# Kernel optimization log

Measured on AMD Instinct MI355X. Metric: run time of the kernel, lower is better.

The kernel has to match this reference:

```python
import jax, jax.numpy as jnp
import numpy as np

OLD = (32, 32)   # fine grid coord_dims
NEW = (16, 16)   # coarse grid (dims // 2)
N_ORDERS = 6     # multi-indices of total order <= 2 in 2 coords


def lin_resize(x, new_size, axis):
    # 1D linear interpolation along `axis`, align_corners=True (matches F.interpolate)
    old = x.shape[axis]
    pos = jnp.arange(new_size, dtype=x.dtype) * ((old - 1) / (new_size - 1))
    lo = jnp.clip(jnp.floor(pos).astype(jnp.int32), 0, old - 2)
    w = pos - lo.astype(x.dtype)
    xl = jnp.take(x, lo, axis=axis)
    xh = jnp.take(x, lo + 1, axis=axis)
    shp = [1] * x.ndim
    shp[axis] = new_size
    w = w.reshape(shp)
    return xl * (1.0 - w) + xh * w


def bilinear_resize(x, new_hw):
    # separable bilinear, align_corners=True; x is [..., H, W]
    x = lin_resize(x, new_hw[0], x.ndim - 2)
    return lin_resize(x, new_hw[1], x.ndim - 1)


def setup_inputs():
    key = jax.random.key(0)
    ks = jax.random.split(key, 6)
    B = 32                      # bs * n_ind_dim = 8 * 4
    G = OLD[0] * OLD[1]         # fine grid size = 1024
    m, n = 2048, 1536           # coarse constraints x coarse vars (16*16*6)
    return {
        "coeffs": jax.random.normal(ks[0], (B, G, N_ORDERS), jnp.float32),
        "rhs": jax.random.normal(ks[1], (B, G), jnp.float32),
        "steps_x": jax.random.uniform(ks[2], (B, OLD[0] - 1), jnp.float32),
        "steps_y": jax.random.uniform(ks[3], (B, OLD[1] - 1), jnp.float32),
        "A": jax.random.normal(ks[4], (B, m, n), jnp.float32) * 0.05,
        "A_rhs": jax.random.normal(ks[5], (B, m), jnp.float32),
    }


def reference(coeffs, rhs, steps_x, steps_y, A, A_rhs):
    B = coeffs.shape[0]
    new_G = NEW[0] * NEW[1]

    # --- downsample_coeffs: [B,G,O] -> [B,O,H,W] -> bilinear -> [B,newG,O]
    c = coeffs.transpose(0, 2, 1).reshape(B, N_ORDERS, OLD[0], OLD[1])
    c = bilinear_resize(c, NEW)
    new_coeffs = c.reshape(B, N_ORDERS, new_G).transpose(0, 2, 1)

    # --- downsample_rhs: [B,G] -> [B,1,H,W] -> bilinear -> [B,newG]
    r = bilinear_resize(rhs.reshape(B, 1, OLD[0], OLD[1]), NEW)
    new_rhs = r.reshape(B, new_G)

    # --- downsample_steps: drop last, pairwise sum
    nsx = steps_x[:, :-1].reshape(B, OLD[0] // 2 - 1, 2).sum(axis=-1)
    nsy = steps_y[:, :-1].reshape(B, OLD[1] // 2 - 1, 2).sum(axis=-1)

    # --- make_AtA (coarsest path: dense bmm) ---
    AtA = jnp.einsum('bmn,bmk->bnk', A, A)           # At @ A, [B,n,n]
    AtPrhs = jnp.einsum('bmn,bm->bn', A, A_rhs)      # At @ rhs
    D = jnp.sum(A * A, axis=1)                       # diag(AtA) = column sums of squares

    # --- L/U split (get_tril): L = cols <= rows, U = cols > rows ---
    n = AtA.shape[-1]
    ridx = jnp.arange(n)
    lmask = ridx[:, None] >= ridx[None, :]
    L = jnp.where(lmask, AtA, jnp.zeros((), AtA.dtype))
    U = jnp.where(lmask, jnp.zeros((), AtA.dtype), AtA)

    return (new_coeffs, new_rhs, nsx, nsy, AtA, AtPrhs, D, L, U)
```

## Files before the change

kernel.cpp:

```cpp
#include <hip/hip_runtime.h>
#include <math.h>

#define NB 32
#define M 2048
#define N 1536
#define NORD 6

#define OFF_COEFFS 0
#define OFF_RHS    49152
#define OFF_NSX    57344
#define OFF_NSY    57824
#define OFF_ATA    58304
#define OFF_ATPRHS 75555776
#define OFF_D      75604928
#define OFF_L      75654080
#define OFF_U      151151552
#define SMALL_TOTAL 58304

typedef short short8v __attribute__((ext_vector_type(8)));
typedef float f32x4 __attribute__((ext_vector_type(4)));

__device__ __forceinline__ void gload16(const void* g, void* l) {
    __builtin_amdgcn_global_load_lds(
        (const __attribute__((address_space(1))) void*)g,
        (__attribute__((address_space(3))) void*)l, 16, 0, 0);
}

__device__ __forceinline__ uint rtn_bf16(float x) {
    uint u = __float_as_uint(x);
    return (u + 0x7fffu + ((u >> 16) & 1u)) >> 16;
}

__device__ __forceinline__ void nts(float v, float* p) {
    __builtin_nontemporal_store(v, p);
}
__device__ __forceinline__ void nts4(f32x4 v, float* p) {
    __builtin_nontemporal_store(v, (f32x4*)p);
}

__global__ void small_kernel(const float* __restrict__ coeffs,
                             const float* __restrict__ rhs,
                             const float* __restrict__ sx,
                             const float* __restrict__ sy,
                             float* __restrict__ out) {
    int idx = blockIdx.x * blockDim.x + threadIdx.x;
    if (idx >= SMALL_TOTAL) return;
    const float scale = 31.0f / 15.0f;
    if (idx < 49152) {
        int b = idx / 1536;
        int rem = idx % 1536;
        int gp = rem / 6;
        int o  = rem % 6;
        int yy = gp / 16, xx = gp % 16;
        float py = (float)yy * scale;
        int ly = (int)floorf(py); if (ly > 30) ly = 30;
        float wy = py - (float)ly;
        float px = (float)xx * scale;
        int lx = (int)floorf(px); if (lx > 30) lx = 30;
        float wx = px - (float)lx;
        const float* base = coeffs + (size_t)b * 1024 * NORD;
        float v00 = base[(ly * 32 + lx) * NORD + o];
        float v01 = base[(ly * 32 + lx + 1) * NORD + o];
        float v10 = base[((ly + 1) * 32 + lx) * NORD + o];
        float v11 = base[((ly + 1) * 32 + lx + 1) * NORD + o];
        float a  = v00 * (1.0f - wy) + v10 * wy;
        float bb = v01 * (1.0f - wy) + v11 * wy;
        out[OFF_COEFFS + idx] = a * (1.0f - wx) + bb * wx;
    } else if (idx < 57344) {
        int j = idx - 49152;
        int b = j / 256;
        int gp = j % 256;
        int yy = gp / 16, xx = gp % 16;
        float py = (float)yy * scale;
        int ly = (int)floorf(py); if (ly > 30) ly = 30;
        float wy = py - (float)ly;
        float px = (float)xx * scale;
        int lx = (int)floorf(px); if (lx > 30) lx = 30;
        float wx = px - (float)lx;
        const float* base = rhs + (size_t)b * 1024;
        float v00 = base[ly * 32 + lx];
        float v01 = base[ly * 32 + lx + 1];
        float v10 = base[(ly + 1) * 32 + lx];
        float v11 = base[(ly + 1) * 32 + lx + 1];
        float a  = v00 * (1.0f - wy) + v10 * wy;
        float bb = v01 * (1.0f - wy) + v11 * wy;
        out[OFF_RHS + j] = a * (1.0f - wx) + bb * wx;
    } else if (idx < 57824) {
        int j = idx - 57344;
        int b = j / 15, k = j % 15;
        out[OFF_NSX + j] = sx[b * 31 + 2 * k] + sx[b * 31 + 2 * k + 1];
    } else {
        int j = idx - 57824;
        int b = j / 15, k = j % 15;
        out[OFF_NSY + j] = sy[b * 31 + 2 * k] + sy[b * 31 + 2 * k + 1];
    }
}

__global__ __launch_bounds__(256) void split_kernel(const float* __restrict__ A,
                                                    const float* __restrict__ Arhs,
                                                    ushort* __restrict__ Ahi,
                                                    float2* __restrict__ part) {
    int bid = blockIdx.x;
    int q  = bid & 3;
    int cb = (bid >> 2) % 6;
    int b  = bid / 24;
    int t  = threadIdx.x;
    int col = cb * 256 + t;
    const float* Ab = A + (size_t)b * M * N;
    const float* rb = Arhs + (size_t)b * M;
    uint4* Hp = (uint4*)Ahi;
    float s1 = 0.0f, s2 = 0.0f;
    for (int oct = q * 64; oct < q * 64 + 64; ++oct) {
        uint hw[4];
#pragma unroll
        for (int j = 0; j < 4; ++j) {
            float a0 = Ab[(size_t)(oct * 8 + 2 * j) * N + col];
            float a1 = Ab[(size_t)(oct * 8 + 2 * j + 1) * N + col];
            float r0 = rb[oct * 8 + 2 * j];
            float r1 = rb[oct * 8 + 2 * j + 1];
            s1 = fmaf(a0, r0, s1); s1 = fmaf(a1, r1, s1);
            s2 = fmaf(a0, a0, s2); s2 = fmaf(a1, a1, s2);
            hw[j] = rtn_bf16(a0) | (rtn_bf16(a1) << 16);
        }
        Hp[(size_t)(b * 256 + oct) * N + col] = make_uint4(hw[0], hw[1], hw[2], hw[3]);
    }
    part[(size_t)q * (NB * 6 * 256) + (size_t)(b * 6 + cb) * 256 + t] = make_float2(s1, s2);
}

__global__ __launch_bounds__(256) void reduce_kernel(const float2* __restrict__ part,
                                                     float* __restrict__ out) {
    int idx = blockIdx.x * 256 + threadIdx.x;
    float s1 = 0.0f, s2 = 0.0f;
#pragma unroll
    for (int q = 0; q < 4; ++q) {
        float2 p = part[(size_t)q * (NB * 6 * 256) + idx];
        s1 += p.x; s2 += p.y;
    }
    out[OFF_ATPRHS + idx] = s1;
    out[OFF_D + idx] = s2;
}

#define SYRK_BLOCKS (NB * 78)

__global__ __launch_bounds__(256, 4) void syrk3_kernel(const ushort* __restrict__ Ahi,
                                                       float* __restrict__ out) {
    __shared__ ushort lds[2][1024 * 8];

    int bid = blockIdx.x;
    int swz = (bid % 8) * (SYRK_BLOCKS / 8) + bid / 8;
    int b = swz / 78;
    int p = swz % 78;
    int ti = 0;
    while ((ti + 1) * (ti + 2) / 2 <= p) ++ti;
    int tj = p - ti * (ti + 1) / 2;
    bool diag = (ti == tj);
    int i0 = ti * 128, j0 = tj * 128;

    int t = threadIdx.x, w = t >> 6, l = t & 63;
    int wr = w >> 1, wc = w & 1;
    int lc = l & 15, lg = l >> 4;

    const ushort* base = Ahi + (size_t)b * 256 * N * 8;

    f32x4 acc[4][4];
#pragma unroll
    for (int i = 0; i < 4; ++i)
#pragma unroll
        for (int j = 0; j < 4; ++j)
#pragma unroll
            for (int k = 0; k < 4; ++k) acc[i][j][k] = 0.0f;

    int nq = diag ? 2 : 4;
    auto stage = [&](int buf, int s) {
        ushort* Lb = &lds[buf][0];
#pragma unroll
        for (int q = 0; q < 4; ++q) {
            if (q < nq) {
                int G = q * 256 + t;
                int arr = G >> 9, oct = (G >> 7) & 3, col = G & 127;
                int colb = arr ? j0 : i0;
                gload16(base + ((size_t)(s * 4 + oct) * N + colb + col) * 8,
                        &Lb[(size_t)G * 8]);
            }
        }
    };

    stage(0, 0);

    int cur = 0;
    for (int s = 0; s < 64; ++s) {
        if (s < 63) {
            stage(cur ^ 1, s + 1);
            if (diag) asm volatile("s_waitcnt vmcnt(2)" ::: "memory");
            else      asm volatile("s_waitcnt vmcnt(4)" ::: "memory");
        } else {
            asm volatile("s_waitcnt vmcnt(0)" ::: "memory");
        }
        __builtin_amdgcn_s_barrier();
        asm volatile("" ::: "memory");

        const ushort* Areg = &lds[cur][0];
        const ushort* Breg = diag ? Areg : (Areg + 512 * 8);
        short8v Bv[4];
#pragma unroll
        for (int bj = 0; bj < 4; ++bj)
            Bv[bj] = *(const short8v*)&Breg[(size_t)(lg * 128 + wc * 64 + bj * 16 + lc) * 8];
        __builtin_amdgcn_s_setprio(1);
#pragma unroll
        for (int ai = 0; ai < 4; ++ai) {
            short8v Av = *(const short8v*)&Areg[(size_t)(lg * 128 + wr * 64 + ai * 16 + lc) * 8];
#pragma unroll
            for (int bj = 0; bj < 4; ++bj)
                acc[ai][bj] = __builtin_amdgcn_mfma_f32_16x16x32_bf16(Av, Bv[bj], acc[ai][bj], 0, 0, 0);
        }
        __builtin_amdgcn_s_setprio(0);

        asm volatile("" ::: "memory");
        __builtin_amdgcn_s_barrier();
        cur ^= 1;
    }

    float* AtA = out + OFF_ATA + (size_t)b * N * N;
    float* Lo  = out + OFF_L   + (size_t)b * N * N;
    float* Up  = out + OFF_U   + (size_t)b * N * N;

#pragma unroll
    for (int ai = 0; ai < 4; ++ai) {
        int gi0 = i0 + wr * 64 + ai * 16 + lg * 4;
#pragma unroll
        for (int bj = 0; bj < 4; ++bj) {
            int gj = j0 + wc * 64 + bj * 16 + lc;
#pragma unroll
            for (int r = 0; r < 4; ++r) {
                int gi = gi0 + r;
                float v = acc[ai][bj][r];
                size_t o = (size_t)gi * N + gj;
                nts(v, AtA + o);
                nts((gj <= gi) ? v : 0.0f, Lo + o);
                nts((gj >  gi) ? v : 0.0f, Up + o);
            }
            if (!diag) {
                f32x4 va = acc[ai][bj], vl, vu;
#pragma unroll
                for (int r = 0; r < 4; ++r) {
                    int gi = gi0 + r;
                    vl[r] = (gi <= gj) ? va[r] : 0.0f;
                    vu[r] = (gi >  gj) ? va[r] : 0.0f;
                }
                size_t om = (size_t)gj * N + gi0;
                nts4(va, AtA + om);
                nts4(vl, Lo  + om);
                nts4(vu, Up  + om);
            }
        }
    }
}

__global__ __launch_bounds__(256) void atp_d_kernel(const float* __restrict__ A,
                                                    const float* __restrict__ Arhs,
                                                    float* __restrict__ out) {
    int b  = blockIdx.x / 6;
    int cb = blockIdx.x % 6;
    int col = cb * 256 + threadIdx.x;
    const float* Ab = A + (size_t)b * M * N;
    const float* rb = Arhs + (size_t)b * M;
    float s1 = 0.0f, s2 = 0.0f;
#pragma unroll 4
    for (int m = 0; m < M; ++m) {
        float a = Ab[(size_t)m * N + col];
        float r = rb[m];
        s1 = fmaf(a, r, s1);
        s2 = fmaf(a, a, s2);
    }
    out[OFF_ATPRHS + b * N + col] = s1;
    out[OFF_D      + b * N + col] = s2;
}

#define BM 128
#define BK 16
#define NPAIRS 78

__global__ __launch_bounds__(256, 2) void syrk_kernel(const float* __restrict__ A,
                                                      float* __restrict__ out) {
    __shared__ float As[BK][BM];
    __shared__ float Bs[BK][BM];

    int bid = blockIdx.x;
    int b = bid / NPAIRS;
    int p = bid % NPAIRS;
    int ti = (int)((sqrtf(8.0f * (float)p + 1.0f) - 1.0f) * 0.5f);
    while ((ti + 1) * (ti + 2) / 2 <= p) ++ti;
    while (ti * (ti + 1) / 2 > p) --ti;
    int tj = p - ti * (ti + 1) / 2;
    int i0 = ti * BM, j0 = tj * BM;

    const float* Ab = A + (size_t)b * M * N;
    int t = threadIdx.x;
    int tx = t % 16, ty = t / 16;
    int lcv = (t % 32) * 4;
    int lk = t / 32;

    float acc[2][4][2][4] = {};

    for (int m0 = 0; m0 < M; m0 += BK) {
        const float* pa = Ab + (size_t)(m0 + lk) * N;
        float4 a0 = *(const float4*)(pa + i0 + lcv);
        float4 a1 = *(const float4*)(pa + (size_t)8 * N + i0 + lcv);
        float4 b0 = *(const float4*)(pa + j0 + lcv);
        float4 b1 = *(const float4*)(pa + (size_t)8 * N + j0 + lcv);
        *(float4*)&As[lk][lcv]     = a0;
        *(float4*)&As[lk + 8][lcv] = a1;
        *(float4*)&Bs[lk][lcv]     = b0;
        *(float4*)&Bs[lk + 8][lcv] = b1;
        __syncthreads();
#pragma unroll
        for (int kk = 0; kk < BK; ++kk) {
            float ar[2][4], br[2][4];
            *(float4*)&ar[0][0] = *(const float4*)&As[kk][ty * 4];
            *(float4*)&ar[1][0] = *(const float4*)&As[kk][64 + ty * 4];
            *(float4*)&br[0][0] = *(const float4*)&Bs[kk][tx * 4];
            *(float4*)&br[1][0] = *(const float4*)&Bs[kk][64 + tx * 4];
#pragma unroll
            for (int rh = 0; rh < 2; ++rh)
#pragma unroll
                for (int r = 0; r < 4; ++r)
#pragma unroll
                    for (int ch = 0; ch < 2; ++ch)
#pragma unroll
                        for (int c = 0; c < 4; ++c)
                            acc[rh][r][ch][c] = fmaf(ar[rh][r], br[ch][c], acc[rh][r][ch][c]);
        }
        __syncthreads();
    }

    float* AtA = out + OFF_ATA + (size_t)b * N * N;
    float* L   = out + OFF_L   + (size_t)b * N * N;
    float* U   = out + OFF_U   + (size_t)b * N * N;

#pragma unroll
    for (int rh = 0; rh < 2; ++rh)
#pragma unroll
        for (int r = 0; r < 4; ++r) {
            int gi = i0 + rh * 64 + ty * 4 + r;
#pragma unroll
            for (int ch = 0; ch < 2; ++ch) {
                int gjb = j0 + ch * 64 + tx * 4;
                float ta[4], tl[4], tu[4];
#pragma unroll
                for (int c = 0; c < 4; ++c) {
                    int gj = gjb + c;
                    float v = acc[rh][r][ch][c];
                    ta[c] = v;
                    tl[c] = (gj <= gi) ? v : 0.0f;
                    tu[c] = (gj >  gi) ? v : 0.0f;
                }
                size_t o = (size_t)gi * N + gjb;
                *(float4*)(AtA + o) = *(float4*)ta;
                *(float4*)(L   + o) = *(float4*)tl;
                *(float4*)(U   + o) = *(float4*)tu;
            }
        }

    if (ti != tj) {
#pragma unroll
        for (int ch = 0; ch < 2; ++ch)
#pragma unroll
            for (int c = 0; c < 4; ++c) {
                int gj = j0 + ch * 64 + tx * 4 + c;
#pragma unroll
                for (int rh = 0; rh < 2; ++rh) {
                    int gib = i0 + rh * 64 + ty * 4;
                    float ta[4], tl[4], tu[4];
#pragma unroll
                    for (int r = 0; r < 4; ++r) {
                        int gi = gib + r;
                        float v = acc[rh][r][ch][c];
                        ta[r] = v;
                        tl[r] = (gi <= gj) ? v : 0.0f;
                        tu[r] = (gi >  gj) ? v : 0.0f;
                    }
                    size_t o = (size_t)gj * N + gib;
                    *(float4*)(AtA + o) = *(float4*)ta;
                    *(float4*)(L   + o) = *(float4*)tl;
                    *(float4*)(U   + o) = *(float4*)tu;
                }
            }
    }
}

extern "C" void kernel_launch(void* const* d_in, const int* in_sizes, int n_in,
                              void* d_out, int out_size, void* d_ws, size_t ws_size,
                              hipStream_t stream) {
    const float* coeffs = (const float*)d_in[0];
    const float* rhs    = (const float*)d_in[1];
    const float* sx     = (const float*)d_in[2];
    const float* sy     = (const float*)d_in[3];
    const float* A      = (const float*)d_in[4];
    const float* Arhs   = (const float*)d_in[5];
    float* out = (float*)d_out;

    small_kernel<<<(SMALL_TOTAL + 255) / 256, 256, 0, stream>>>(coeffs, rhs, sx, sy, out);

    const size_t hi_bytes   = (size_t)NB * M * N * sizeof(ushort);
    const size_t part_bytes = (size_t)4 * NB * 6 * 256 * sizeof(float2);
    if (ws_size >= hi_bytes + part_bytes) {
        ushort* Ahi  = (ushort*)d_ws;
        float2* part = (float2*)((char*)d_ws + hi_bytes);
        split_kernel<<<768, 256, 0, stream>>>(A, Arhs, Ahi, part);
        reduce_kernel<<<192, 256, 0, stream>>>(part, out);
        syrk3_kernel<<<SYRK_BLOCKS, 256, 0, stream>>>(Ahi, out);
    } else {
        atp_d_kernel<<<NB * 6, 256, 0, stream>>>(A, Arhs, out);
        syrk_kernel<<<NB * NPAIRS, 256, 0, stream>>>(A, out);
    }
}
```

Before: 550.9 us.

## Load SYRK operands directly into registers, dropping LDS staging and barriers

The SYRK kernel no longer stages A tiles through LDS with global_load_lds and double-buffered barriers. Each wave now loads its own bf16 fragments straight from global memory into registers, with two register buffers for prefetch, and occupancy is lowered to 2 blocks per CU. This removes LDS traffic and barrier synchronisation. In exchange, tiles shared between waves are read redundantly from global memory or cache, diagonal tiles lose their single-load sharing, and register pressure rises.

New measurement: 633.1 us. 1.15x slower.

```diff
diff --git a/kernel.cpp b/kernel.cpp
--- a/kernel.cpp
+++ b/kernel.cpp
@@ -19,12 +19,6 @@
 
 typedef short short8v __attribute__((ext_vector_type(8)));
 typedef float f32x4 __attribute__((ext_vector_type(4)));
-
-__device__ __forceinline__ void gload16(const void* g, void* l) {
-    __builtin_amdgcn_global_load_lds(
-        (const __attribute__((address_space(1))) void*)g,
-        (__attribute__((address_space(3))) void*)l, 16, 0, 0);
-}
 
 __device__ __forceinline__ uint rtn_bf16(float x) {
     uint u = __float_as_uint(x);
@@ -140,14 +134,13 @@
     out[OFF_D + idx] = s2;
 }
 
-#define SYRK_BLOCKS (NB * 78)
-
-__global__ __launch_bounds__(256, 4) void syrk3_kernel(const ushort* __restrict__ Ahi,
+#define SYRKR_BLOCKS (NB * 78)
+#define KSTRIDE (4 * N * 16)
+
+__global__ __launch_bounds__(256, 2) void syrkr_kernel(const ushort* __restrict__ Ahi,
                                                        float* __restrict__ out) {
-    __shared__ ushort lds[2][1024 * 8];
-
     int bid = blockIdx.x;
-    int swz = (bid % 8) * (SYRK_BLOCKS / 8) + bid / 8;
+    int swz = (bid % 8) * (SYRKR_BLOCKS / 8) + bid / 8;
     int b = swz / 78;
     int p = swz % 78;
     int ti = 0;
@@ -160,7 +153,9 @@
     int wr = w >> 1, wc = w & 1;
     int lc = l & 15, lg = l >> 4;
 
-    const ushort* base = Ahi + (size_t)b * 256 * N * 8;
+    const char* base = (const char*)(Ahi + (size_t)b * 256 * N * 8);
+    const char* pa = base + ((size_t)lg * N + i0 + wr * 64 + lc) * 16;
+    const char* pb = base + ((size_t)lg * N + j0 + wc * 64 + lc) * 16;
 
     f32x4 acc[4][4];
 #pragma unroll
@@ -170,55 +165,54 @@
 #pragma unroll
             for (int k = 0; k < 4; ++k) acc[i][j][k] = 0.0f;
 
-    int nq = diag ? 2 : 4;
-    auto stage = [&](int buf, int s) {
-        ushort* Lb = &lds[buf][0];
-#pragma unroll
-        for (int q = 0; q < 4; ++q) {
-            if (q < nq) {
-                int G = q * 256 + t;
-                int arr = G >> 9, oct = (G >> 7) & 3, col = G & 127;
-                int colb = arr ? j0 : i0;
-                gload16(base + ((size_t)(s * 4 + oct) * N + colb + col) * 8,
-                        &Lb[(size_t)G * 8]);
-            }
-        }
-    };
-
-    stage(0, 0);
-
-    int cur = 0;
-    for (int s = 0; s < 64; ++s) {
-        if (s < 63) {
-            stage(cur ^ 1, s + 1);
-            if (diag) asm volatile("s_waitcnt vmcnt(2)" ::: "memory");
-            else      asm volatile("s_waitcnt vmcnt(4)" ::: "memory");
-        } else {
-            asm volatile("s_waitcnt vmcnt(0)" ::: "memory");
-        }
-        __builtin_amdgcn_s_barrier();
-        asm volatile("" ::: "memory");
-
-        const ushort* Areg = &lds[cur][0];
-        const ushort* Breg = diag ? Areg : (Areg + 512 * 8);
-        short8v Bv[4];
+    short8v A0[4], B0[4], A1[4], B1[4];
+#pragma unroll
+    for (int i = 0; i < 4; ++i) {
+        A0[i] = *(const short8v*)(pa + i * 256);
+        B0[i] = *(const short8v*)(pb + i * 256);
+        A1[i] = *(const short8v*)(pa + KSTRIDE + i * 256);
+        B1[i] = *(const short8v*)(pb + KSTRIDE + i * 256);
+    }
+    const char* paN  = pa + 2 * (size_t)KSTRIDE;
+    const char* pbN  = pb + 2 * (size_t)KSTRIDE;
+    const char* paN1 = pa + 3 * (size_t)KSTRIDE;
+    const char* pbN1 = pb + 3 * (size_t)KSTRIDE;
+
+    for (int s = 0; s < 62; s += 2) {
+#pragma unroll
+        for (int ai = 0; ai < 4; ++ai)
+#pragma unroll
+            for (int bj = 0; bj < 4; ++bj)
+                acc[ai][bj] = __builtin_amdgcn_mfma_f32_16x16x32_bf16(A0[ai], B0[bj], acc[ai][bj], 0, 0, 0);
+#pragma unroll
+        for (int i = 0; i < 4; ++i) {
+            A0[i] = *(const short8v*)(paN + i * 256);
+            B0[i] = *(const short8v*)(pbN + i * 256);
+        }
+        paN += 2 * (size_t)KSTRIDE; pbN += 2 * (size_t)KSTRIDE;
+
+#pragma unroll
+        for (int ai = 0; ai < 4; ++ai)
+#pragma unroll
+            for (int bj = 0; bj < 4; ++bj)
+                acc[ai][bj] = __builtin_amdgcn_mfma_f32_16x16x32_bf16(A1[ai], B1[bj], acc[ai][bj], 0, 0, 0);
+#pragma unroll
+        for (int i = 0; i < 4; ++i) {
+            A1[i] = *(const short8v*)(paN1 + i * 256);
+            B1[i] = *(const short8v*)(pbN1 + i * 256);
+        }
+        paN1 += 2 * (size_t)KSTRIDE; pbN1 += 2 * (size_t)KSTRIDE;
+    }
+#pragma unroll
+    for (int ai = 0; ai < 4; ++ai)
 #pragma unroll
         for (int bj = 0; bj < 4; ++bj)
-            Bv[bj] = *(const short8v*)&Breg[(size_t)(lg * 128 + wc * 64 + bj * 16 + lc) * 8];
-        __builtin_amdgcn_s_setprio(1);
-#pragma unroll
-        for (int ai = 0; ai < 4; ++ai) {
-            short8v Av = *(const short8v*)&Areg[(size_t)(lg * 128 + wr * 64 + ai * 16 + lc) * 8];
-#pragma unroll
-            for (int bj = 0; bj < 4; ++bj)
-                acc[ai][bj] = __builtin_amdgcn_mfma_f32_16x16x32_bf16(Av, Bv[bj], acc[ai][bj], 0, 0, 0);
-        }
-        __builtin_amdgcn_s_setprio(0);
-
-        asm volatile("" ::: "memory");
-        __builtin_amdgcn_s_barrier();
-        cur ^= 1;
-    }
+            acc[ai][bj] = __builtin_amdgcn_mfma_f32_16x16x32_bf16(A0[ai], B0[bj], acc[ai][bj], 0, 0, 0);
+#pragma unroll
+    for (int ai = 0; ai < 4; ++ai)
+#pragma unroll
+        for (int bj = 0; bj < 4; ++bj)
+            acc[ai][bj] = __builtin_amdgcn_mfma_f32_16x16x32_bf16(A1[ai], B1[bj], acc[ai][bj], 0, 0, 0);
 
     float* AtA = out + OFF_ATA + (size_t)b * N * N;
     float* Lo  = out + OFF_L   + (size_t)b * N * N;
@@ -408,7 +402,7 @@
         float2* part = (float2*)((char*)d_ws + hi_bytes);
         split_kernel<<<768, 256, 0, stream>>>(A, Arhs, Ahi, part);
         reduce_kernel<<<192, 256, 0, stream>>>(part, out);
-        syrk3_kernel<<<SYRK_BLOCKS, 256, 0, stream>>>(Ahi, out);
+        syrkr_kernel<<<SYRKR_BLOCKS, 256, 0, stream>>>(Ahi, out);
     } else {
         atp_d_kernel<<<NB * 6, 256, 0, stream>>>(A, Arhs, out);
         syrk_kernel<<<NB * NPAIRS, 256, 0, stream>>>(A, out);
```
